# Performance work log

Hardware: AMD Instinct MI355X
Metric: run time of the kernel (lower is better)

Reference implementation:

```python
import jax, jax.numpy as jnp
import numpy as np


def setup_inputs() -> dict:
    key = jax.random.key(0)
    ks = jax.random.split(key, 6)
    B = 16
    return {
        "concat_gap": jax.random.normal(ks[0], (B, 448), dtype=jnp.float32),
        "out1": jax.random.normal(ks[1], (B, 64, 15, 64, 64), dtype=jnp.float32),
        "out2": jax.random.normal(ks[2], (B, 128, 8, 32, 32), dtype=jnp.float32),
        "out3": jax.random.normal(ks[3], (B, 256, 4, 16, 16), dtype=jnp.float32),
        "weight": jax.random.normal(ks[4], (3, 448), dtype=jnp.float32) * 0.05,
        "bias": jax.random.normal(ks[5], (3,), dtype=jnp.float32) * 0.05,
    }


def _vis(out, w_covid, w_cap):
    # fused channel-wise weighted reduction: (sum_c out[:,c]*w0[c] + sum_c out[:,c]*w1[c]) / 2
    w = (w_covid + w_cap) * 0.5  # [C]
    v = jnp.einsum('bcdhw,c->bdhw', out, w)
    return v[:, None]  # [B,1,D,H,W]


def reference(concat_gap, out1, out2, out3, weight, bias):
    # fc_out = addmm(bias, concat_gap, weight.T)
    fc_out = concat_gap @ weight.T + bias  # [B,3]
    vis1 = _vis(out1, weight[0, :64], weight[1, :64])
    vis2 = _vis(out2, weight[0, 64:192], weight[1, 64:192])
    vis3 = _vis(out3, weight[0, 192:448], weight[1, 192:448])
    return (fc_out, vis1, vis2, vis3)
```

## Files before the change

kernel.cpp:

```cpp
#include <hip/hip_runtime.h>


typedef float fvec4 __attribute__((ext_vector_type(4)));

__device__ __forceinline__ fvec4 ntload(const fvec4* p) {
    return __builtin_nontemporal_load(p);
}
__device__ __forceinline__ void ntstore(fvec4* p, fvec4 v) {
    __builtin_nontemporal_store(v, p);
}

__global__ __launch_bounds__(256) void fused_vis_fc_v2(
    const float* __restrict__ concat_gap,
    const float* __restrict__ out1,
    const float* __restrict__ out2,
    const float* __restrict__ out3,
    const float* __restrict__ weight,
    const float* __restrict__ bias,
    float* __restrict__ d_out)
{
    const int t = threadIdx.x;
    int blk = blockIdx.x;

    __shared__ float s_w[256];
    __shared__ fvec4 s_red[128];

    if (blk < 32) {
        const int b    = blk >> 1;
        const int s4   = ((blk & 1) << 7) + (t & 127);
        const int half = t >> 7;
        for (int c = t; c < 256; c += 256)
            s_w[c] = 0.5f * (weight[192 + c] + weight[640 + c]);
        __syncthreads();

        const fvec4* in4 = (const fvec4*)out3
            + (size_t)b * 256 * 256 + (size_t)(half * 128) * 256 + s4;
        fvec4 acc = {0.f, 0.f, 0.f, 0.f};
        #pragma unroll 8
        for (int c = 0; c < 128; ++c)
            acc += ntload(in4 + (size_t)c * 256) * s_w[half * 128 + c];

        if (half) s_red[t & 127] = acc;
        __syncthreads();
        if (!half) {
            acc += s_red[t];
            ntstore((fvec4*)(d_out + 48 + 983040 + 131072) + b * 256 + s4, acc);
        }
    } else if (blk < 160) {
        blk -= 32;
        const int b  = blk >> 3;
        const int s4 = ((blk & 7) << 8) + t;
        for (int c = t; c < 128; c += 256)
            s_w[c] = 0.5f * (weight[64 + c] + weight[512 + c]);
        __syncthreads();

        const fvec4* in4 = (const fvec4*)out2 + (size_t)b * 128 * 2048 + s4;
        fvec4 acc = {0.f, 0.f, 0.f, 0.f};
        #pragma unroll 8
        for (int c = 0; c < 128; ++c)
            acc += ntload(in4 + (size_t)c * 2048) * s_w[c];
        ntstore((fvec4*)(d_out + 48 + 983040) + b * 2048 + s4, acc);
    } else if (blk < 640) {
        blk -= 160;
        const int b     = blk / 30;
        const int chunk = (blk % 30) * 512;
        for (int c = t; c < 64; c += 256)
            s_w[c] = 0.5f * (weight[c] + weight[448 + c]);
        __syncthreads();

        const fvec4* in4 = (const fvec4*)out1
            + (size_t)b * 64 * 15360 + chunk + t;
        fvec4 a0 = {0.f, 0.f, 0.f, 0.f};
        fvec4 a1 = {0.f, 0.f, 0.f, 0.f};
        #pragma unroll 8
        for (int c = 0; c < 64; ++c) {
            const float w = s_w[c];
            a0 += ntload(in4 + (size_t)c * 15360) * w;
            a1 += ntload(in4 + (size_t)c * 15360 + 256) * w;
        }
        fvec4* o = (fvec4*)(d_out + 48) + (size_t)b * 15360 + chunk + t;
        ntstore(o, a0);
        ntstore(o + 256, a1);
    } else {
        if (t < 48) {
            const int b = t / 3, o = t % 3;
            const float* g = concat_gap + b * 448;
            const float* w = weight + o * 448;
            float s = 0.f;
            #pragma unroll 8
            for (int k = 0; k < 448; ++k) s += g[k] * w[k];
            d_out[t] = s + bias[o];
        }
    }
}

extern "C" void kernel_launch(void* const* d_in, const int* in_sizes, int n_in,
                              void* d_out, int out_size, void* d_ws, size_t ws_size,
                              hipStream_t stream) {
    fused_vis_fc_v2<<<641, 256, 0, stream>>>(
        (const float*)d_in[0], (const float*)d_in[1], (const float*)d_in[2],
        (const float*)d_in[3], (const float*)d_in[4], (const float*)d_in[5],
        (float*)d_out);
}
```

Measured before the change: 370.4 us.

## Split channel reduction into partial-sum pass plus separate reduce kernel

Splits the channel dimension into groups so that more blocks stream the large inputs in parallel. Each block writes partial sums to workspace, and a second kernel adds the partials and writes the final outputs. The aim is more memory-level parallelism across the device. In exchange it adds workspace write and read traffic (a large extra amount of data for out1) and a second kernel launch.

Result: no change. 377.7 us (+2.0%).

```diff
diff --git a/kernel.cpp b/kernel.cpp
--- a/kernel.cpp
+++ b/kernel.cpp
@@ -2,6 +2,9 @@
 
 
 typedef float fvec4 __attribute__((ext_vector_type(4)));
+
+#define W2_OFF 983040
+#define W3_OFF 1114112
 
 __device__ __forceinline__ fvec4 ntload(const fvec4* p) {
     return __builtin_nontemporal_load(p);
@@ -10,77 +13,78 @@
     __builtin_nontemporal_store(v, p);
 }
 
-__global__ __launch_bounds__(256) void fused_vis_fc_v2(
+__global__ __launch_bounds__(256) void pass1_partials(
     const float* __restrict__ concat_gap,
     const float* __restrict__ out1,
     const float* __restrict__ out2,
     const float* __restrict__ out3,
     const float* __restrict__ weight,
     const float* __restrict__ bias,
-    float* __restrict__ d_out)
+    float* __restrict__ d_out,
+    fvec4* __restrict__ ws)
 {
     const int t = threadIdx.x;
-    int blk = blockIdx.x;
+    const int blk = blockIdx.x;
+    __shared__ float s_w[128];
 
-    __shared__ float s_w[256];
-    __shared__ fvec4 s_red[128];
-
-    if (blk < 32) {
-        const int b    = blk >> 1;
-        const int s4   = ((blk & 1) << 7) + (t & 127);
-        const int half = t >> 7;
-        for (int c = t; c < 256; c += 256)
-            s_w[c] = 0.5f * (weight[192 + c] + weight[640 + c]);
+    if (blk < 128) {
+        const int b = blk >> 3, r = blk & 7, chunk = r >> 2, cg = r & 3;
+        if (t < 32) {
+            const int c = cg * 32 + t;
+            s_w[t] = 0.5f * (weight[64 + c] + weight[512 + c]);
+        }
         __syncthreads();
-
-        const fvec4* in4 = (const fvec4*)out3
-            + (size_t)b * 256 * 256 + (size_t)(half * 128) * 256 + s4;
-        fvec4 acc = {0.f, 0.f, 0.f, 0.f};
+        const fvec4* in = (const fvec4*)out2
+            + (size_t)(b * 128 + cg * 32) * 2048 + chunk * 1024 + t;
+        fvec4 a0 = {0,0,0,0}, a1 = {0,0,0,0}, a2 = {0,0,0,0}, a3 = {0,0,0,0};
+        #pragma unroll 4
+        for (int cc = 0; cc < 32; ++cc) {
+            const float w = s_w[cc];
+            const fvec4* p = in + (size_t)cc * 2048;
+            a0 += ntload(p)       * w;
+            a1 += ntload(p + 256) * w;
+            a2 += ntload(p + 512) * w;
+            a3 += ntload(p + 768) * w;
+        }
+        fvec4* o = ws + W2_OFF + (size_t)((b * 2 + chunk) * 4 + cg) * 1024 + t;
+        o[0] = a0; o[256] = a1; o[512] = a2; o[768] = a3;
+    } else if (blk < 160) {
+        const int id = blk - 128;
+        const int b = id >> 1, cg = id & 1;
+        if (t < 128) {
+            const int c = cg * 128 + t;
+            s_w[t] = 0.5f * (weight[192 + c] + weight[640 + c]);
+        }
+        __syncthreads();
+        const fvec4* in = (const fvec4*)out3 + (size_t)(b * 256 + cg * 128) * 256 + t;
+        fvec4 acc = {0,0,0,0};
         #pragma unroll 8
-        for (int c = 0; c < 128; ++c)
-            acc += ntload(in4 + (size_t)c * 256) * s_w[half * 128 + c];
-
-        if (half) s_red[t & 127] = acc;
-        __syncthreads();
-        if (!half) {
-            acc += s_red[t];
-            ntstore((fvec4*)(d_out + 48 + 983040 + 131072) + b * 256 + s4, acc);
+        for (int cc = 0; cc < 128; ++cc)
+            acc += ntload(in + (size_t)cc * 256) * s_w[cc];
+        ws[W3_OFF + (b * 2 + cg) * 256 + t] = acc;
+    } else if (blk < 1120) {
+        const int id = blk - 160;
+        const int b = id / 60, r = id % 60, chunk = r >> 2, cg = r & 3;
+        float wr[16];
+        #pragma unroll
+        for (int j = 0; j < 16; ++j) {
+            const int c = cg * 16 + j;
+            wr[j] = 0.5f * (weight[c] + weight[448 + c]);
         }
-    } else if (blk < 160) {
-        blk -= 32;
-        const int b  = blk >> 3;
-        const int s4 = ((blk & 7) << 8) + t;
-        for (int c = t; c < 128; c += 256)
-            s_w[c] = 0.5f * (weight[64 + c] + weight[512 + c]);
-        __syncthreads();
-
-        const fvec4* in4 = (const fvec4*)out2 + (size_t)b * 128 * 2048 + s4;
-        fvec4 acc = {0.f, 0.f, 0.f, 0.f};
-        #pragma unroll 8
-        for (int c = 0; c < 128; ++c)
-            acc += ntload(in4 + (size_t)c * 2048) * s_w[c];
-        ntstore((fvec4*)(d_out + 48 + 983040) + b * 2048 + s4, acc);
-    } else if (blk < 640) {
-        blk -= 160;
-        const int b     = blk / 30;
-        const int chunk = (blk % 30) * 512;
-        for (int c = t; c < 64; c += 256)
-            s_w[c] = 0.5f * (weight[c] + weight[448 + c]);
-        __syncthreads();
-
-        const fvec4* in4 = (const fvec4*)out1
-            + (size_t)b * 64 * 15360 + chunk + t;
-        fvec4 a0 = {0.f, 0.f, 0.f, 0.f};
-        fvec4 a1 = {0.f, 0.f, 0.f, 0.f};
-        #pragma unroll 8
-        for (int c = 0; c < 64; ++c) {
-            const float w = s_w[c];
-            a0 += ntload(in4 + (size_t)c * 15360) * w;
-            a1 += ntload(in4 + (size_t)c * 15360 + 256) * w;
+        const fvec4* in = (const fvec4*)out1
+            + (size_t)(b * 64 + cg * 16) * 15360 + chunk * 1024 + t;
+        fvec4 a0 = {0,0,0,0}, a1 = {0,0,0,0}, a2 = {0,0,0,0}, a3 = {0,0,0,0};
+        #pragma unroll 4
+        for (int cc = 0; cc < 16; ++cc) {
+            const float w = wr[cc];
+            const fvec4* p = in + (size_t)cc * 15360;
+            a0 += ntload(p)       * w;
+            a1 += ntload(p + 256) * w;
+            a2 += ntload(p + 512) * w;
+            a3 += ntload(p + 768) * w;
         }
-        fvec4* o = (fvec4*)(d_out + 48) + (size_t)b * 15360 + chunk + t;
-        ntstore(o, a0);
-        ntstore(o + 256, a1);
+        fvec4* o = ws + (size_t)((b * 15 + chunk) * 4 + cg) * 1024 + t;
+        o[0] = a0; o[256] = a1; o[512] = a2; o[768] = a3;
     } else {
         if (t < 48) {
             const int b = t / 3, o = t % 3;
@@ -94,11 +98,37 @@
     }
 }
 
+__global__ __launch_bounds__(256) void pass2_reduce(
+    const fvec4* __restrict__ ws,
+    float* __restrict__ d_out)
+{
+    const int gid = blockIdx.x * 256 + threadIdx.x;
+    fvec4* o4 = (fvec4*)d_out;
+    if (gid < 245760) {
+        const int b = gid / 15360, within = gid % 15360;
+        const int chunk = within >> 10, s = within & 1023;
+        const fvec4* p = ws + (size_t)(b * 15 + chunk) * 4096 + s;
+        ntstore(o4 + 12 + gid, p[0] + p[1024] + p[2048] + p[3072]);
+    } else if (gid < 278528) {
+        const int g2 = gid - 245760;
+        const int b = g2 >> 11, within = g2 & 2047;
+        const int chunk = within >> 10, s = within & 1023;
+        const fvec4* p = ws + W2_OFF + (size_t)(b * 2 + chunk) * 4096 + s;
+        ntstore(o4 + 245772 + g2, p[0] + p[1024] + p[2048] + p[3072]);
+    } else {
+        const int g3 = gid - 278528;
+        const int b = g3 >> 8, s = g3 & 255;
+        const fvec4* p = ws + W3_OFF + b * 512 + s;
+        ntstore(o4 + 278540 + g3, p[0] + p[256]);
+    }
+}
+
 extern "C" void kernel_launch(void* const* d_in, const int* in_sizes, int n_in,
                               void* d_out, int out_size, void* d_ws, size_t ws_size,
                               hipStream_t stream) {
-    fused_vis_fc_v2<<<641, 256, 0, stream>>>(
+    pass1_partials<<<1121, 256, 0, stream>>>(
         (const float*)d_in[0], (const float*)d_in[1], (const float*)d_in[2],
         (const float*)d_in[3], (const float*)d_in[4], (const float*)d_in[5],
-        (float*)d_out);
+        (float*)d_out, (fvec4*)d_ws);
+    pass2_reduce<<<1104, 256, 0, stream>>>((const fvec4*)d_ws, (float*)d_out);
 }
```
